# Kernel optimization log

Hardware: AMD Instinct MI355X
Metric: run time of the kernel (lower is better)

## Reference

```python
import jax, jax.numpy as jnp
import numpy as np

HIDDEN = 32


def setup_inputs() -> dict:
    key = jax.random.key(0)
    ks = jax.random.split(key, 8)
    B, T, I = 1024, 512, 64
    s_ih = 1.0 / np.sqrt(HIDDEN)
    return {
        "x": jax.random.normal(ks[0], (B, T, I), dtype=jnp.float32),
        "h0": jnp.zeros((1, B, HIDDEN), dtype=jnp.float32),
        "W_ih": jax.random.uniform(ks[1], (HIDDEN, I), jnp.float32, -s_ih, s_ih),
        "b_ih": jax.random.uniform(ks[2], (HIDDEN,), jnp.float32, -s_ih, s_ih),
        "W_hh": jax.random.uniform(ks[3], (HIDDEN, HIDDEN), jnp.float32, -s_ih, s_ih),
        "b_hh": jax.random.uniform(ks[4], (HIDDEN,), jnp.float32, -s_ih, s_ih),
        "W_out": jax.random.uniform(ks[5], (1, HIDDEN), jnp.float32, -s_ih, s_ih),
        "b_out": jax.random.uniform(ks[6], (1,), jnp.float32, -s_ih, s_ih),
    }


def reference(x, h0, W_ih, b_ih, W_hh, b_hh, W_out, b_out):
    # x: [B, T, I]; h0: [1, B, H] (num_layers=1)
    # Precompute input contribution for all timesteps in one GEMM: [B, T, H]
    x_proj = jnp.einsum("bti,hi->bth", x, W_ih) + b_ih

    def step(h, xt):  # h: [B, H], xt: [B, H]
        h_new = jnp.tanh(xt + h @ W_hh.T + b_hh)
        return h_new, h_new

    h_last, r_out_t = jax.lax.scan(step, h0[0], jnp.swapaxes(x_proj, 0, 1))
    r_out = jnp.swapaxes(r_out_t, 0, 1)  # [B, T, H]
    # Per-timestep Linear(32 -> 1), batched as one GEMM: [B, T, 1]
    outs = r_out @ W_out.T + b_out
    return outs, h_last[None]
```

## Files before the change

kernel.cpp:

```cpp
#include <hip/hip_runtime.h>

#define Bc 1024
#define Tc 512
#define Ic 64
#define Hc 32
#define XP 516

typedef __bf16 bf16x8 __attribute__((ext_vector_type(8)));
typedef __bf16 bf16x4 __attribute__((ext_vector_type(4)));
typedef float  f32x4  __attribute__((ext_vector_type(4)));

__device__ inline bf16x8 to_bf16x8(float4 u0, float4 u1) {
    bf16x8 t;
    t[0] = (__bf16)u0.x; t[1] = (__bf16)u0.y; t[2] = (__bf16)u0.z; t[3] = (__bf16)u0.w;
    t[4] = (__bf16)u1.x; t[5] = (__bf16)u1.y; t[6] = (__bf16)u1.z; t[7] = (__bf16)u1.w;
    return t;
}

#define RWC(hvv, wvv)                                                         \
    a0 = fmaf((hvv).x, (wvv).x, a0);                                          \
    a1 = fmaf((hvv).y, (wvv).y, a1);                                          \
    a2 = fmaf((hvv).z, (wvv).z, a2);                                          \
    a3 = fmaf((hvv).w, (wvv).w, a3);

#define STEP(xval, uu)                                                        \
    {                                                                         \
        hbuf[half][h] = hval;                                                 \
        __builtin_amdgcn_wave_barrier();                                      \
        const float4* hv = (const float4*)hbuf[half];                         \
        const float4 h0v = hv[0], h1v = hv[1], h2v = hv[2], h3v = hv[3],      \
                     h4v = hv[4], h5v = hv[5], h6v = hv[6], h7v = hv[7];      \
        float a0 = (xval) + bias, a1 = 0.f, a2 = 0.f, a3 = 0.f;               \
        RWC(h0v, w0) RWC(h1v, w1) RWC(h2v, w2) RWC(h3v, w3)                   \
        RWC(h4v, w4) RWC(h5v, w5) RWC(h6v, w6) RWC(h7v, w7)                   \
        const float a = (a0 + a1) + (a2 + a3);                                \
        const float p  = __builtin_amdgcn_exp2f(a * 2.8853900817779268f);     \
        const float rr = __builtin_amdgcn_rcpf(p + 1.0f);                     \
        hval = fmaf(-2.0f, rr, 1.0f);                                         \
        pbuf[half][uu][h] = wo * hval;                                        \
        __builtin_amdgcn_wave_barrier();                                      \
    }

#define CVT4(dst, src)                                                        \
    dst.x = (float)(src)[0]; dst.y = (float)(src)[1];                         \
    dst.z = (float)(src)[2]; dst.w = (float)(src)[3];

__global__ __launch_bounds__(64) void fused_rnn_kernel(
    const float* __restrict__ x, const float* __restrict__ Wih,
    const float* __restrict__ bih, const float* __restrict__ h0,
    const float* __restrict__ Whh, const float* __restrict__ bhh,
    const float* __restrict__ Wout, const float* __restrict__ bout,
    float* __restrict__ out)
{
    __shared__ __bf16 xq[2][Hc][XP];
    __shared__ float hbuf[2][32];
    __shared__ float pbuf[2][16][34];

    const int lane = threadIdx.x;
    const int half = lane >> 5;
    const int h    = lane & 31;
    const int m    = lane & 15;
    const int q    = lane >> 4;
    const int b0   = blockIdx.x * 2;

    bf16x8 Bf[2][2];
#pragma unroll
    for (int nh = 0; nh < 2; ++nh)
#pragma unroll
        for (int kh = 0; kh < 2; ++kh) {
            const float* wp = Wih + (m + 16 * nh) * Ic + q * 8 + kh * 32;
            Bf[nh][kh] = to_bf16x8(((const float4*)wp)[0], ((const float4*)wp)[1]);
        }
    const float bias0 = bih[m];
    const float bias1 = bih[m + 16];

#pragma unroll 4
    for (int tt = 0; tt < 64; ++tt) {
        const int bb = tt >> 5;
        const int lt = tt & 31;
        const float* xp0 =
            x + ((size_t)(b0 + bb) * Tc + lt * 16 + m) * Ic + q * 8;
        const bf16x8 A0 = to_bf16x8(((const float4*)xp0)[0],
                                    ((const float4*)xp0)[1]);
        const bf16x8 A1 = to_bf16x8(((const float4*)(xp0 + 32))[0],
                                    ((const float4*)(xp0 + 32))[1]);

        f32x4 acc0 = {0.f, 0.f, 0.f, 0.f};
        f32x4 acc1 = {0.f, 0.f, 0.f, 0.f};
        acc0 = __builtin_amdgcn_mfma_f32_16x16x32_bf16(A0, Bf[0][0], acc0, 0, 0, 0);
        acc0 = __builtin_amdgcn_mfma_f32_16x16x32_bf16(A1, Bf[0][1], acc0, 0, 0, 0);
        acc1 = __builtin_amdgcn_mfma_f32_16x16x32_bf16(A0, Bf[1][0], acc1, 0, 0, 0);
        acc1 = __builtin_amdgcn_mfma_f32_16x16x32_bf16(A1, Bf[1][1], acc1, 0, 0, 0);

        bf16x4 p0, p1;
        p0[0] = (__bf16)(acc0[0] + bias0); p0[1] = (__bf16)(acc0[1] + bias0);
        p0[2] = (__bf16)(acc0[2] + bias0); p0[3] = (__bf16)(acc0[3] + bias0);
        p1[0] = (__bf16)(acc1[0] + bias1); p1[1] = (__bf16)(acc1[1] + bias1);
        p1[2] = (__bf16)(acc1[2] + bias1); p1[3] = (__bf16)(acc1[3] + bias1);
        *(bf16x4*)&xq[bb][m][lt * 16 + q * 4]      = p0;
        *(bf16x4*)&xq[bb][m + 16][lt * 16 + q * 4] = p1;
    }

    __syncthreads();

    const float4* wrow = (const float4*)(Whh + h * Hc);
    const float4 w0 = wrow[0], w1 = wrow[1], w2 = wrow[2], w3 = wrow[3],
                 w4 = wrow[4], w5 = wrow[5], w6 = wrow[6], w7 = wrow[7];
    const float bias = bhh[h];
    const float wo   = Wout[h];
    const float bo   = bout[0];

    float hval = h0[(size_t)(b0 + half) * Hc + h];
    float* orow = out + (size_t)(b0 + half) * Tc;

    const __bf16* xrow = &xq[half][h][0];

    bf16x4 r0 = *(const bf16x4*)(xrow + 0), r1 = *(const bf16x4*)(xrow + 4),
           r2 = *(const bf16x4*)(xrow + 8), r3 = *(const bf16x4*)(xrow + 12);
    float4 q0, q1, q2, q3;
    CVT4(q0, r0) CVT4(q1, r1) CVT4(q2, r2) CVT4(q3, r3)

    for (int tb = 0; tb < Tc / 16; ++tb) {
        const int tbn = (tb + 1 < Tc / 16) ? tb + 1 : tb;
        const __bf16* nx = xrow + tbn * 16;
        const bf16x4 m0 = *(const bf16x4*)(nx + 0),
                     m1 = *(const bf16x4*)(nx + 4),
                     m2 = *(const bf16x4*)(nx + 8),
                     m3 = *(const bf16x4*)(nx + 12);

        STEP(q0.x, 0)  STEP(q0.y, 1)  STEP(q0.z, 2)  STEP(q0.w, 3)
        STEP(q1.x, 4)  STEP(q1.y, 5)  STEP(q1.z, 6)  STEP(q1.w, 7)
        STEP(q2.x, 8)  STEP(q2.y, 9)  STEP(q2.z, 10) STEP(q2.w, 11)
        STEP(q3.x, 12) STEP(q3.y, 13) STEP(q3.z, 14) STEP(q3.w, 15)

        __builtin_amdgcn_wave_barrier();

        if (h < 16) {
            const float2* pr = (const float2*)pbuf[half][h];
            float2 sa = pr[0], sb = pr[1];
#pragma unroll
            for (int mm = 2; mm < 16; mm += 2) {
                sa.x += pr[mm].x;     sa.y += pr[mm].y;
                sb.x += pr[mm + 1].x; sb.y += pr[mm + 1].y;
            }
            orow[tb * 16 + h] = ((sa.x + sb.x) + (sa.y + sb.y)) + bo;
        }
        __builtin_amdgcn_wave_barrier();

        CVT4(q0, m0) CVT4(q1, m1) CVT4(q2, m2) CVT4(q3, m3)
    }

    out[(size_t)Bc * Tc + (size_t)(b0 + half) * Hc + h] = hval;
}

extern "C" void kernel_launch(void* const* d_in, const int* in_sizes, int n_in,
                              void* d_out, int out_size, void* d_ws, size_t ws_size,
                              hipStream_t stream) {
    const float* x    = (const float*)d_in[0];
    const float* h0   = (const float*)d_in[1];
    const float* Wih  = (const float*)d_in[2];
    const float* bih  = (const float*)d_in[3];
    const float* Whh  = (const float*)d_in[4];
    const float* bhh  = (const float*)d_in[5];
    const float* Wout = (const float*)d_in[6];
    const float* bout = (const float*)d_in[7];
    float* out = (float*)d_out;

    fused_rnn_kernel<<<Bc / 2, 64, 0, stream>>>(x, Wih, bih, h0, Whh, bhh,
                                                Wout, bout, out);
}
```

Baseline: 275.5 us.

## Interleave input projection with recurrence and use fp16 mixed-FMA hidden state

Moves the x·W_ih MFMA projection from a separate prologue into the recurrent loop, software-pipelining global loads and MFMA two and three tiles ahead so memory latency overlaps the serial recurrence. Reparameterizes tanh as r=1/(1+exp2(a)), folding the log2e scale and the -2 factor into the weights and bias so each step drops a multiply and an FMA. Stores the recurrent state as fp16 in LDS and uses v_fma_mix_f32 so one dword read carries two hidden values, halving LDS traffic per step. This trades precision, since the hidden state is rounded to fp16, and it relies on inline asm.

Result: faster. 244.4 us (-11.3%).

```diff
diff --git a/kernel.cpp b/kernel.cpp
--- a/kernel.cpp
+++ b/kernel.cpp
@@ -5,6 +5,7 @@
 #define Ic 64
 #define Hc 32
 #define XP 516
+#define LOG2E2 2.8853900817779268f
 
 typedef __bf16 bf16x8 __attribute__((ext_vector_type(8)));
 typedef __bf16 bf16x4 __attribute__((ext_vector_type(4)));
@@ -16,34 +17,83 @@
     t[4] = (__bf16)u1.x; t[5] = (__bf16)u1.y; t[6] = (__bf16)u1.z; t[7] = (__bf16)u1.w;
     return t;
 }
-
-#define RWC(hvv, wvv)                                                         \
-    a0 = fmaf((hvv).x, (wvv).x, a0);                                          \
-    a1 = fmaf((hvv).y, (wvv).y, a1);                                          \
-    a2 = fmaf((hvv).z, (wvv).z, a2);                                          \
-    a3 = fmaf((hvv).w, (wvv).w, a3);
+__device__ inline bf16x8 to_bf16x8s(float4 u0, float4 u1, float s) {
+    bf16x8 t;
+    t[0] = (__bf16)(u0.x*s); t[1] = (__bf16)(u0.y*s); t[2] = (__bf16)(u0.z*s); t[3] = (__bf16)(u0.w*s);
+    t[4] = (__bf16)(u1.x*s); t[5] = (__bf16)(u1.y*s); t[6] = (__bf16)(u1.z*s); t[7] = (__bf16)(u1.w*s);
+    return t;
+}
+
+
+#define FMIX_LO(acc, hw, wf)                                                  \
+    asm("v_fma_mix_f32 %0, %1, %2, %0 op_sel:[0,0,0] op_sel_hi:[1,0,0]"       \
+        : "+v"(acc) : "v"(hw), "v"(wf));
+#define FMIX_HI(acc, hw, wf)                                                  \
+    asm("v_fma_mix_f32 %0, %1, %2, %0 op_sel:[1,0,0] op_sel_hi:[1,0,0]"       \
+        : "+v"(acc) : "v"(hw), "v"(wf));
 
 #define STEP(xval, uu)                                                        \
     {                                                                         \
-        hbuf[half][h] = hval;                                                 \
+        hbuf[half][h] = rv;                                                   \
         __builtin_amdgcn_wave_barrier();                                      \
-        const float4* hv = (const float4*)hbuf[half];                         \
-        const float4 h0v = hv[0], h1v = hv[1], h2v = hv[2], h3v = hv[3],      \
-                     h4v = hv[4], h5v = hv[5], h6v = hv[6], h7v = hv[7];      \
-        float a0 = (xval) + bias, a1 = 0.f, a2 = 0.f, a3 = 0.f;               \
-        RWC(h0v, w0) RWC(h1v, w1) RWC(h2v, w2) RWC(h3v, w3)                   \
-        RWC(h4v, w4) RWC(h5v, w5) RWC(h6v, w6) RWC(h7v, w7)                   \
-        const float a = (a0 + a1) + (a2 + a3);                                \
-        const float p  = __builtin_amdgcn_exp2f(a * 2.8853900817779268f);     \
-        const float rr = __builtin_amdgcn_rcpf(p + 1.0f);                     \
-        hval = fmaf(-2.0f, rr, 1.0f);                                         \
-        pbuf[half][uu][h] = wo * hval;                                        \
+        const uint4 Ha = hq[0], Hb = hq[1], Hc2 = hq[2], Hd2 = hq[3];         \
+        float a0 = (xval) + biasc, a1 = 0.f, a2 = 0.f, a3 = 0.f;              \
+        FMIX_LO(a0, Ha.x, w0.x)  FMIX_HI(a1, Ha.x, w0.y)                      \
+        FMIX_LO(a2, Ha.y, w0.z)  FMIX_HI(a3, Ha.y, w0.w)                      \
+        FMIX_LO(a0, Ha.z, w1.x)  FMIX_HI(a1, Ha.z, w1.y)                      \
+        FMIX_LO(a2, Ha.w, w1.z)  FMIX_HI(a3, Ha.w, w1.w)                      \
+        FMIX_LO(a0, Hb.x, w2.x)  FMIX_HI(a1, Hb.x, w2.y)                      \
+        FMIX_LO(a2, Hb.y, w2.z)  FMIX_HI(a3, Hb.y, w2.w)                      \
+        FMIX_LO(a0, Hb.z, w3.x)  FMIX_HI(a1, Hb.z, w3.y)                      \
+        FMIX_LO(a2, Hb.w, w3.z)  FMIX_HI(a3, Hb.w, w3.w)                      \
+        FMIX_LO(a0, Hc2.x, w4.x) FMIX_HI(a1, Hc2.x, w4.y)                     \
+        FMIX_LO(a2, Hc2.y, w4.z) FMIX_HI(a3, Hc2.y, w4.w)                     \
+        FMIX_LO(a0, Hc2.z, w5.x) FMIX_HI(a1, Hc2.z, w5.y)                     \
+        FMIX_LO(a2, Hc2.w, w5.z) FMIX_HI(a3, Hc2.w, w5.w)                     \
+        FMIX_LO(a0, Hd2.x, w6.x) FMIX_HI(a1, Hd2.x, w6.y)                     \
+        FMIX_LO(a2, Hd2.y, w6.z) FMIX_HI(a3, Hd2.y, w6.w)                     \
+        FMIX_LO(a0, Hd2.z, w7.x) FMIX_HI(a1, Hd2.z, w7.y)                     \
+        FMIX_LO(a2, Hd2.w, w7.z) FMIX_HI(a3, Hd2.w, w7.w)                     \
+        const float a_ = (a0 + a1) + (a2 + a3);                               \
+        const float p_ = __builtin_amdgcn_exp2f(a_);                          \
+        rr = __builtin_amdgcn_rcpf(p_ + 1.0f);                                \
+        rv = (_Float16)rr;                                                    \
+        pbuf[half][uu][h] = fmaf(rr, w2o, wo);                                \
         __builtin_amdgcn_wave_barrier();                                      \
     }
 
 #define CVT4(dst, src)                                                        \
     dst.x = (float)(src)[0]; dst.y = (float)(src)[1];                         \
     dst.z = (float)(src)[2]; dst.w = (float)(src)[3];
+
+#define TILE_LOAD(Xn, bb, lt)                                                 \
+    do {                                                                      \
+        const float* xp_ =                                                    \
+            x + ((size_t)(b0 + (bb)) * Tc + (lt) * 16 + m) * Ic + q * 8;      \
+        Xn##0 = ((const float4*)xp_)[0];                                      \
+        Xn##1 = ((const float4*)xp_)[1];                                      \
+        Xn##2 = ((const float4*)(xp_ + 32))[0];                               \
+        Xn##3 = ((const float4*)(xp_ + 32))[1];                               \
+    } while (0)
+
+#define TILE_MFMA(Xn, bb, lt)                                                 \
+    do {                                                                      \
+        const bf16x8 A0_ = to_bf16x8(Xn##0, Xn##1);                           \
+        const bf16x8 A1_ = to_bf16x8(Xn##2, Xn##3);                           \
+        f32x4 ac0 = {0.f, 0.f, 0.f, 0.f};                                     \
+        f32x4 ac1 = {0.f, 0.f, 0.f, 0.f};                                     \
+        ac0 = __builtin_amdgcn_mfma_f32_16x16x32_bf16(A0_, Bf[0][0], ac0, 0, 0, 0); \
+        ac0 = __builtin_amdgcn_mfma_f32_16x16x32_bf16(A1_, Bf[0][1], ac0, 0, 0, 0); \
+        ac1 = __builtin_amdgcn_mfma_f32_16x16x32_bf16(A0_, Bf[1][0], ac1, 0, 0, 0); \
+        ac1 = __builtin_amdgcn_mfma_f32_16x16x32_bf16(A1_, Bf[1][1], ac1, 0, 0, 0); \
+        bf16x4 p0_, p1_;                                                      \
+        p0_[0] = (__bf16)(ac0[0] + bias0); p0_[1] = (__bf16)(ac0[1] + bias0); \
+        p0_[2] = (__bf16)(ac0[2] + bias0); p0_[3] = (__bf16)(ac0[3] + bias0); \
+        p1_[0] = (__bf16)(ac1[0] + bias1); p1_[1] = (__bf16)(ac1[1] + bias1); \
+        p1_[2] = (__bf16)(ac1[2] + bias1); p1_[3] = (__bf16)(ac1[3] + bias1); \
+        *(bf16x4*)&xq[bb][m][(lt) * 16 + q * 4]      = p0_;                   \
+        *(bf16x4*)&xq[bb][m + 16][(lt) * 16 + q * 4] = p1_;                   \
+    } while (0)
 
 __global__ __launch_bounds__(64) void fused_rnn_kernel(
     const float* __restrict__ x, const float* __restrict__ Wih,
@@ -52,9 +102,9 @@
     const float* __restrict__ Wout, const float* __restrict__ bout,
     float* __restrict__ out)
 {
-    __shared__ __bf16 xq[2][Hc][XP];
-    __shared__ float hbuf[2][32];
-    __shared__ float pbuf[2][16][34];
+    __shared__ __bf16   xq[2][Hc][XP];
+    __shared__ _Float16 hbuf[2][32];
+    __shared__ float    pbuf[2][16][34];
 
     const int lane = threadIdx.x;
     const int half = lane >> 5;
@@ -69,57 +119,56 @@
 #pragma unroll
         for (int kh = 0; kh < 2; ++kh) {
             const float* wp = Wih + (m + 16 * nh) * Ic + q * 8 + kh * 32;
-            Bf[nh][kh] = to_bf16x8(((const float4*)wp)[0], ((const float4*)wp)[1]);
+            Bf[nh][kh] = to_bf16x8s(((const float4*)wp)[0],
+                                    ((const float4*)wp)[1], LOG2E2);
         }
-    const float bias0 = bih[m];
-    const float bias1 = bih[m + 16];
-
-#pragma unroll 4
-    for (int tt = 0; tt < 64; ++tt) {
-        const int bb = tt >> 5;
-        const int lt = tt & 31;
-        const float* xp0 =
-            x + ((size_t)(b0 + bb) * Tc + lt * 16 + m) * Ic + q * 8;
-        const bf16x8 A0 = to_bf16x8(((const float4*)xp0)[0],
-                                    ((const float4*)xp0)[1]);
-        const bf16x8 A1 = to_bf16x8(((const float4*)(xp0 + 32))[0],
-                                    ((const float4*)(xp0 + 32))[1]);
-
-        f32x4 acc0 = {0.f, 0.f, 0.f, 0.f};
-        f32x4 acc1 = {0.f, 0.f, 0.f, 0.f};
-        acc0 = __builtin_amdgcn_mfma_f32_16x16x32_bf16(A0, Bf[0][0], acc0, 0, 0, 0);
-        acc0 = __builtin_amdgcn_mfma_f32_16x16x32_bf16(A1, Bf[0][1], acc0, 0, 0, 0);
-        acc1 = __builtin_amdgcn_mfma_f32_16x16x32_bf16(A0, Bf[1][0], acc1, 0, 0, 0);
-        acc1 = __builtin_amdgcn_mfma_f32_16x16x32_bf16(A1, Bf[1][1], acc1, 0, 0, 0);
-
-        bf16x4 p0, p1;
-        p0[0] = (__bf16)(acc0[0] + bias0); p0[1] = (__bf16)(acc0[1] + bias0);
-        p0[2] = (__bf16)(acc0[2] + bias0); p0[3] = (__bf16)(acc0[3] + bias0);
-        p1[0] = (__bf16)(acc1[0] + bias1); p1[1] = (__bf16)(acc1[1] + bias1);
-        p1[2] = (__bf16)(acc1[2] + bias1); p1[3] = (__bf16)(acc1[3] + bias1);
-        *(bf16x4*)&xq[bb][m][lt * 16 + q * 4]      = p0;
-        *(bf16x4*)&xq[bb][m + 16][lt * 16 + q * 4] = p1;
-    }
-
-    __syncthreads();
+    const float bias0 = bih[m] * LOG2E2;
+    const float bias1 = bih[m + 16] * LOG2E2;
 
     const float4* wrow = (const float4*)(Whh + h * Hc);
-    const float4 w0 = wrow[0], w1 = wrow[1], w2 = wrow[2], w3 = wrow[3],
-                 w4 = wrow[4], w5 = wrow[5], w6 = wrow[6], w7 = wrow[7];
-    const float bias = bhh[h];
-    const float wo   = Wout[h];
-    const float bo   = bout[0];
-
-    float hval = h0[(size_t)(b0 + half) * Hc + h];
+    float4 t0 = wrow[0], t1 = wrow[1], t2 = wrow[2], t3 = wrow[3],
+           t4 = wrow[4], t5 = wrow[5], t6 = wrow[6], t7 = wrow[7];
+    const float rsum =
+        (((t0.x + t0.y) + (t0.z + t0.w)) + ((t1.x + t1.y) + (t1.z + t1.w))) +
+        (((t2.x + t2.y) + (t2.z + t2.w)) + ((t3.x + t3.y) + (t3.z + t3.w))) +
+        (((t4.x + t4.y) + (t4.z + t4.w)) + ((t5.x + t5.y) + (t5.z + t5.w))) +
+        (((t6.x + t6.y) + (t6.z + t6.w)) + ((t7.x + t7.y) + (t7.z + t7.w)));
+    const float cw = -2.0f * LOG2E2;
+    float4 w0, w1, w2, w3, w4, w5, w6, w7;
+    w0.x = t0.x*cw; w0.y = t0.y*cw; w0.z = t0.z*cw; w0.w = t0.w*cw;
+    w1.x = t1.x*cw; w1.y = t1.y*cw; w1.z = t1.z*cw; w1.w = t1.w*cw;
+    w2.x = t2.x*cw; w2.y = t2.y*cw; w2.z = t2.z*cw; w2.w = t2.w*cw;
+    w3.x = t3.x*cw; w3.y = t3.y*cw; w3.z = t3.z*cw; w3.w = t3.w*cw;
+    w4.x = t4.x*cw; w4.y = t4.y*cw; w4.z = t4.z*cw; w4.w = t4.w*cw;
+    w5.x = t5.x*cw; w5.y = t5.y*cw; w5.z = t5.z*cw; w5.w = t5.w*cw;
+    w6.x = t6.x*cw; w6.y = t6.y*cw; w6.z = t6.z*cw; w6.w = t6.w*cw;
+    w7.x = t7.x*cw; w7.y = t7.y*cw; w7.z = t7.z*cw; w7.w = t7.w*cw;
+    const float biasc = (bhh[h] + rsum) * LOG2E2;
+    const float wo  = Wout[h];
+    const float w2o = -2.0f * wo;
+    const float bo  = bout[0];
+
+    float rr = fmaf(-0.5f, h0[(size_t)(b0 + half) * Hc + h], 0.5f);
+    _Float16 rv = (_Float16)rr;
     float* orow = out + (size_t)(b0 + half) * Tc;
 
+    float4 Xa0, Xa1, Xa2, Xa3, Xb0, Xb1, Xb2, Xb3;
+    TILE_LOAD(Xa, 0, 0);  TILE_LOAD(Xb, 1, 0);
+    TILE_MFMA(Xa, 0, 0);  TILE_MFMA(Xb, 1, 0);
+    TILE_LOAD(Xa, 0, 1);  TILE_LOAD(Xb, 1, 1);
+    TILE_MFMA(Xa, 0, 1);  TILE_MFMA(Xb, 1, 1);
+    TILE_LOAD(Xa, 0, 2);  TILE_LOAD(Xb, 1, 2);
+    __builtin_amdgcn_wave_barrier();
+
     const __bf16* xrow = &xq[half][h][0];
+    const uint4*  hq   = (const uint4*)&hbuf[half][0];
 
     bf16x4 r0 = *(const bf16x4*)(xrow + 0), r1 = *(const bf16x4*)(xrow + 4),
            r2 = *(const bf16x4*)(xrow + 8), r3 = *(const bf16x4*)(xrow + 12);
     float4 q0, q1, q2, q3;
     CVT4(q0, r0) CVT4(q1, r1) CVT4(q2, r2) CVT4(q3, r3)
 
+#pragma unroll 1
     for (int tb = 0; tb < Tc / 16; ++tb) {
         const int tbn = (tb + 1 < Tc / 16) ? tb + 1 : tb;
         const __bf16* nx = xrow + tbn * 16;
@@ -127,6 +176,9 @@
                      m1 = *(const bf16x4*)(nx + 4),
                      m2 = *(const bf16x4*)(nx + 8),
                      m3 = *(const bf16x4*)(nx + 12);
+
+        if (tb + 2 < Tc / 16) { TILE_MFMA(Xa, 0, tb + 2); TILE_MFMA(Xb, 1, tb + 2); }
+        if (tb + 3 < Tc / 16) { TILE_LOAD(Xa, 0, tb + 3); TILE_LOAD(Xb, 1, tb + 3); }
 
         STEP(q0.x, 0)  STEP(q0.y, 1)  STEP(q0.z, 2)  STEP(q0.w, 3)
         STEP(q1.x, 4)  STEP(q1.y, 5)  STEP(q1.z, 6)  STEP(q1.w, 7)
@@ -150,7 +202,7 @@
         CVT4(q0, m0) CVT4(q1, m1) CVT4(q2, m2) CVT4(q3, m3)
     }
 
-    out[(size_t)Bc * Tc + (size_t)(b0 + half) * Hc + h] = hval;
+    out[(size_t)Bc * Tc + (size_t)(b0 + half) * Hc + h] = fmaf(-2.0f, rr, 1.0f);
 }
 
 extern "C" void kernel_launch(void* const* d_in, const int* in_sizes, int n_in,
```
